# Kernel optimization log

Hardware: AMD Instinct MI355X
Metric: run time of the kernel (lower is better)

## Reference

```python
import jax, jax.numpy as jnp
import numpy as np

D_MODEL = 192
D_STATE = 128
D_CONV = 4
EXPAND = 2
D_INNER = EXPAND * D_MODEL            # 384
D_HALF = D_INNER // 2                 # 192 (x and z channel count)
DT_RANK = -(-D_MODEL // 16)           # ceil(192/16) = 12
B, H, W = 8, 32, 32


def serpentine(x):
    # flip every odd row along width: x (b, c, h, w)
    return x.at[:, :, 1::2, :].set(jnp.flip(x[:, :, 1::2, :], axis=3))


def causal_dwconv_silu(x, w):
    # x: (b, d, l), w: (d, k). Left-pad -> causal depthwise conv, then silu.
    k = w.shape[1]
    L = x.shape[-1]
    xp = jnp.pad(x, ((0, 0), (0, 0), (k - 1, 0)))
    y = jnp.zeros_like(x)
    for i in range(k):  # k=4, tiny fixed loop
        y = y + w[:, i][None, :, None] * xp[:, :, i:i + L]
    return jax.nn.silu(y)


def selective_scan(u, delta, A, Bm, Cm, Dp):
    # u, delta: (b, d, l); Bm, Cm: (b, n, l); A: (d, n); Dp: (d,)
    b, d, L = u.shape
    n = A.shape[1]

    def step(h, xs):
        u_t, dt_t, B_t, C_t = xs  # (b,d), (b,d), (b,n), (b,n)
        dA = jnp.exp(dt_t[:, :, None] * A)                      # (b,d,n)
        h = dA * h + (dt_t * u_t)[:, :, None] * B_t[:, None, :]
        y = jnp.einsum('bdn,bn->bd', h, C_t)
        return h, y

    xs = (jnp.moveaxis(u, 2, 0), jnp.moveaxis(delta, 2, 0),
          jnp.moveaxis(Bm, 2, 0), jnp.moveaxis(Cm, 2, 0))
    h0 = jnp.zeros((b, d, n), u.dtype)
    _, ys = jax.lax.scan(step, h0, xs)                          # (l, b, d)
    return jnp.moveaxis(ys, 0, 2).reshape(b, d, L) + Dp[None, :, None] * u


def setup_inputs() -> dict:
    key = jax.random.key(0)
    ks = jax.random.split(key, 8)
    hidden_states = jax.random.normal(ks[0], (B, D_MODEL, H, W), jnp.float32)
    W_in = jax.random.normal(ks[1], (D_INNER, D_MODEL), jnp.float32) * 0.02
    conv_w_x = jax.random.normal(ks[2], (D_HALF, D_CONV), jnp.float32) * 0.2
    conv_w_z = jax.random.normal(ks[3], (D_HALF, D_CONV), jnp.float32) * 0.2
    W_xproj = jax.random.normal(ks[4], (DT_RANK + 2 * D_STATE, D_HALF), jnp.float32) * 0.02
    dt_std = DT_RANK ** (-0.5)
    W_dt = jax.random.uniform(ks[5], (D_HALF, DT_RANK), jnp.float32, -dt_std, dt_std)
    # inv-softplus init of dt bias, as in the module
    dt = jnp.exp(jax.random.uniform(ks[6], (D_HALF,), jnp.float32)
                 * (np.log(0.1) - np.log(0.001)) + np.log(0.001))
    dt = jnp.clip(dt, 1e-4, None)
    b_dt = dt + jnp.log(-jnp.expm1(-dt))
    A_log = jnp.log(jnp.broadcast_to(jnp.arange(1, D_STATE + 1, dtype=jnp.float32),
                                     (D_HALF, D_STATE)))
    D_param = jnp.ones((D_HALF,), jnp.float32)
    W_out = jax.random.normal(ks[7], (D_MODEL, D_INNER), jnp.float32) * 0.02
    return {"hidden_states": hidden_states, "W_in": W_in, "conv_w_x": conv_w_x,
            "conv_w_z": conv_w_z, "W_xproj": W_xproj, "W_dt": W_dt, "b_dt": b_dt,
            "A_log": A_log, "D_param": D_param, "W_out": W_out}


def reference(hidden_states, W_in, conv_w_x, conv_w_z, W_xproj, W_dt, b_dt,
              A_log, D_param, W_out):
    b, c, h, w = hidden_states.shape
    L = h * w
    hs = serpentine(hidden_states)
    hs = hs.reshape(b, c, L).transpose(0, 2, 1)                 # (b, l, c)
    xz = hs @ W_in.T                                            # (b, l, 2d)
    xz = xz.transpose(0, 2, 1)                                  # (b, 2d, l)
    x, z = xz[:, :D_HALF], xz[:, D_HALF:]
    A = -jnp.exp(A_log.astype(jnp.float32))                     # (d, n)
    x = causal_dwconv_silu(x, conv_w_x)
    z = causal_dwconv_silu(z, conv_w_z)
    x_dbl = x.transpose(0, 2, 1) @ W_xproj.T                    # (b, l, r+2n)
    dt = x_dbl[..., :DT_RANK]
    Bm = x_dbl[..., DT_RANK:DT_RANK + D_STATE].transpose(0, 2, 1)  # (b, n, l)
    Cm = x_dbl[..., DT_RANK + D_STATE:].transpose(0, 2, 1)         # (b, n, l)
    dt = (dt @ W_dt.T + b_dt).transpose(0, 2, 1)                # (b, d, l), bias once
    # module passes delta_bias=dt_proj.bias again with delta_softplus=True
    delta = jax.nn.softplus(dt + b_dt[None, :, None])           # bias twice, faithful
    y = selective_scan(x, delta, A, Bm, Cm, D_param.astype(jnp.float32))
    y = jnp.concatenate([y, z], axis=1)                         # (b, 2d, l)
    out = y.transpose(0, 2, 1) @ W_out.T                        # (b, l, c)
    out = out.transpose(0, 2, 1).reshape(b, c, h, w)
    return serpentine(out)
```

## Files before the change

kernel.cpp:

```cpp
#include <hip/hip_runtime.h>
#include <math.h>

#define NB  8
#define DM  192
#define DH  192
#define DI  384
#define DS  128
#define DTR 12
#define XR  268
#define L   1024
#define NC  16
#define CL  64
#define NWX 320
#define LOG2E 1.44269504f

__device__ __forceinline__ void wave_lds_sync() {
  __builtin_amdgcn_wave_barrier();
  asm volatile("s_waitcnt lgkmcnt(0)" ::: "memory");
  __builtin_amdgcn_sched_barrier(0);
}

__global__ void k_wt_all(const float* __restrict__ Win,
                         const float* __restrict__ Wx,
                         const float* __restrict__ Wout,
                         float* __restrict__ wt_in,
                         float* __restrict__ wt_x,
                         float* __restrict__ wt_out) {
  const int j = blockIdx.x * 256 + threadIdx.x;
  const int k = blockIdx.y;
  const int z = blockIdx.z;
  if (z == 0) {
    if (k < 192 && j < 384) wt_in[(size_t)k * 384 + j] = Win[(size_t)j * 192 + k];
  } else if (z == 1) {
    if (k < 192 && j < NWX) wt_x[(size_t)k * NWX + j] = (j < XR) ? Wx[(size_t)j * 192 + k] : 0.f;
  } else {
    if (k < 384 && j < 192) wt_out[(size_t)k * 192 + j] = Wout[(size_t)j * 384 + k];
  }
}

template<int K, int N, int NW, int SERP_IN, int OMODE, int DODT>
__global__ __launch_bounds__(256) void k_gemm(const float* __restrict__ A,
                                              const float* __restrict__ Wt,
                                              float* __restrict__ Out,
                                              const float* __restrict__ Wdt,
                                              const float* __restrict__ bdt,
                                              float* __restrict__ dlt) {
  __shared__ float At[32][64];
  const int lane = threadIdx.x & 63;
  const int wv   = threadIdx.x >> 6;
  const int l    = blockIdx.x * 64 + lane;
  const int n0   = __builtin_amdgcn_readfirstlane(blockIdx.y * 64 + wv * 16);
  const int b    = blockIdx.z;
  int lg = l;
  if (SERP_IN || OMODE == 2) {
    int h = l >> 5, w = l & 31;
    lg = h * 32 + ((h & 1) ? (31 - w) : w);
  }
  const float* Ab = A + (size_t)b * K * L + (SERP_IN ? lg : l);
  float acc[16];
#pragma unroll
  for (int i = 0; i < 16; ++i) acc[i] = 0.f;

  for (int k0 = 0; k0 < K; k0 += 32) {
#pragma unroll
    for (int i = 0; i < 8; ++i) {
      int kr = wv * 8 + i;
      At[kr][lane] = Ab[(size_t)(k0 + kr) * L];
    }
    __syncthreads();
#pragma unroll
    for (int kk = 0; kk < 32; ++kk) {
      float a = At[kk][lane];
      const float* wr = Wt + (size_t)(k0 + kk) * NW + n0;
#pragma unroll
      for (int i = 0; i < 16; ++i) acc[i] = fmaf(wr[i], a, acc[i]);
    }
    __syncthreads();
  }

  if (OMODE == 0) {
    float* o = Out + ((size_t)b * N + n0) * L + l;
#pragma unroll
    for (int i = 0; i < 16; ++i) o[(size_t)i * L] = acc[i];
  } else if (OMODE == 1) {
    float* o = Out + ((size_t)b * L + l) * XR;
#pragma unroll
    for (int i = 0; i < 16; i += 4) {
      if (n0 + i + 4 <= XR)
        *(float4*)(o + n0 + i) = make_float4(acc[i], acc[i + 1], acc[i + 2], acc[i + 3]);
    }
    if (DODT && n0 == 0) {
      for (int d = 0; d < DH; ++d) {
        const float* wd = Wdt + d * DTR;
        float s = 2.f * bdt[d];
#pragma unroll
        for (int r = 0; r < DTR; ++r) s = fmaf(wd[r], acc[r], s);
        float v = (s > 20.f) ? s : __logf(1.f + __expf(s));
        dlt[((size_t)b * DH + d) * L + l] = v;
      }
    }
  } else {
    float* o = Out + ((size_t)b * N + n0) * L + lg;
#pragma unroll
    for (int i = 0; i < 16; ++i) o[(size_t)i * L] = acc[i];
  }
}

__global__ void k_conv_silu(const float* __restrict__ xz,
                            const float* __restrict__ cwx,
                            const float* __restrict__ cwz,
                            float* __restrict__ u,
                            float* __restrict__ ycat) {
  int idx = blockIdx.x * blockDim.x + threadIdx.x;
  const int per = NB * DH * (L / 4);
  int part = idx / per;
  int rem  = idx - part * per;
  int l4 = (rem & (L / 4 - 1)) * 4;
  int bd = rem >> 8;
  int d  = bd % DH;
  int b  = bd / DH;
  const float* cw = (part ? cwz : cwx) + d * 4;
  float w0 = cw[0], w1 = cw[1], w2 = cw[2], w3 = cw[3];
  const float* src = xz + ((size_t)b * DI + (part ? DH + d : d)) * L;
  float4 cur = *(const float4*)(src + l4);
  float pm3 = 0.f, pm2 = 0.f, pm1 = 0.f;
  if (l4 >= 4) {
    float4 p = *(const float4*)(src + l4 - 4);
    pm3 = p.y; pm2 = p.z; pm1 = p.w;
  }
  float s0 = fmaf(w3, cur.x, fmaf(w2, pm1,   fmaf(w1, pm2,   w0 * pm3)));
  float s1 = fmaf(w3, cur.y, fmaf(w2, cur.x, fmaf(w1, pm1,   w0 * pm2)));
  float s2 = fmaf(w3, cur.z, fmaf(w2, cur.y, fmaf(w1, cur.x, w0 * pm1)));
  float s3 = fmaf(w3, cur.w, fmaf(w2, cur.z, fmaf(w1, cur.y, w0 * cur.x)));
  float4 y;
  y.x = s0 / (1.f + __expf(-s0));
  y.y = s1 / (1.f + __expf(-s1));
  y.z = s2 / (1.f + __expf(-s2));
  y.w = s3 / (1.f + __expf(-s3));
  float* dst = part ? (ycat + ((size_t)b * DI + DH + d) * L + l4)
                    : (u + (size_t)bd * L + l4);
  *(float4*)dst = y;
}

__global__ void __launch_bounds__(256) k_scan1(const float* __restrict__ xdbl,
                                               const float* __restrict__ delta,
                                               const float* __restrict__ u,
                                               const float* __restrict__ Alog,
                                               float* __restrict__ hpart,
                                               float* __restrict__ apart) {
  __shared__ __align__(16) float dd[4][64][8];
  const int lane = threadIdx.x & 63;
  const int wv   = threadIdx.x >> 6;
  const int d0   = blockIdx.x * 8 + wv * 2;
  const int c = blockIdx.y, b = blockIdx.z;
  const int bd0 = b * DH + d0, bd1 = bd0 + 1;
  const float a00 = -__expf(Alog[(size_t)d0 * DS + 2 * lane]) * LOG2E;
  const float a10 = -__expf(Alog[(size_t)(d0 + 1) * DS + 2 * lane]) * LOG2E;
  const float* xrow  = xdbl + ((size_t)b * L + c * CL) * XR + DTR + 2 * lane;
  const float* drow0 = delta + (size_t)bd0 * L + c * CL;
  const float* drow1 = delta + (size_t)bd1 * L + c * CL;
  const float* urow0 = u + (size_t)bd0 * L + c * CL;
  const float* urow1 = u + (size_t)bd1 * L + c * CL;
  float dt0 = drow0[lane], u0 = urow0[lane];
  float dt1 = drow1[lane], u1 = urow1[lane];
  *(float4*)&dd[wv][lane][0] =
      make_float4(dt0, dt0 * u0, __builtin_amdgcn_exp2f(-dt0 * LOG2E), 0.f);
  *(float4*)&dd[wv][lane][4] =
      make_float4(dt1, dt1 * u1, __builtin_amdgcn_exp2f(-dt1 * LOG2E), 0.f);
  float s0 = dt0, s1 = dt1;
#pragma unroll
  for (int m = 1; m < 64; m <<= 1) {
    s0 += __shfl_xor(s0, m, 64);
    s1 += __shfl_xor(s1, m, 64);
  }
  wave_lds_sync();
  float h00 = 0.f, h01 = 0.f, h10 = 0.f, h11 = 0.f;
#pragma unroll 8
  for (int t = 0; t < CL; ++t) {
    float4 v0 = *(const float4*)&dd[wv][t][0];
    float4 v1 = *(const float4*)&dd[wv][t][4];
    float2 Bv = *(const float2*)(xrow + (size_t)t * XR);
    float e00 = __builtin_amdgcn_exp2f(v0.x * a00);
    float e01 = e00 * v0.z;
    float e10 = __builtin_amdgcn_exp2f(v1.x * a10);
    float e11 = e10 * v1.z;
    h00 = fmaf(e00, h00, v0.y * Bv.x);
    h01 = fmaf(e01, h01, v0.y * Bv.y);
    h10 = fmaf(e10, h10, v1.y * Bv.x);
    h11 = fmaf(e11, h11, v1.y * Bv.y);
  }
  float ap00 = __builtin_amdgcn_exp2f(s0 * a00);
  float ap01 = ap00 * __builtin_amdgcn_exp2f(-s0 * LOG2E);
  float ap10 = __builtin_amdgcn_exp2f(s1 * a10);
  float ap11 = ap10 * __builtin_amdgcn_exp2f(-s1 * LOG2E);
  *(float2*)(hpart + ((size_t)bd0 * NC + c) * 128 + 2 * lane) = make_float2(h00, h01);
  *(float2*)(hpart + ((size_t)bd1 * NC + c) * 128 + 2 * lane) = make_float2(h10, h11);
  *(float2*)(apart + ((size_t)bd0 * NC + c) * 128 + 2 * lane) = make_float2(ap00, ap01);
  *(float2*)(apart + ((size_t)bd1 * NC + c) * 128 + 2 * lane) = make_float2(ap10, ap11);
}

__global__ void __launch_bounds__(64) k_scan2(float* __restrict__ hpart,
                                              const float* __restrict__ apart) {
  const int bd   = blockIdx.x;
  const int lane = threadIdx.x;
  float H1 = 0.f, H2 = 0.f;
  size_t base = (size_t)bd * (NC * 128) + lane;
  for (int c = 0; c < NC; ++c) {
    size_t o = base + c * 128;
    float hp1 = hpart[o], hp2 = hpart[o + 64];
    float ap1 = apart[o], ap2 = apart[o + 64];
    hpart[o] = H1; hpart[o + 64] = H2;
    H1 = fmaf(ap1, H1, hp1);
    H2 = fmaf(ap2, H2, hp2);
  }
}

__global__ void __launch_bounds__(256) k_scan3(const float* __restrict__ xdbl,
                                               const float* __restrict__ delta,
                                               const float* __restrict__ u,
                                               const float* __restrict__ Alog,
                                               const float* __restrict__ Dp,
                                               const float* __restrict__ hin,
                                               float* __restrict__ ycat) {
  __shared__ __align__(16) float dd[4][64][8];
  __shared__ __align__(16) float pbuf[4][2][8][68];
  const int lane = threadIdx.x & 63;
  const int wv   = threadIdx.x >> 6;
  const int d0   = blockIdx.x * 8 + wv * 2;
  const int c = blockIdx.y, b = blockIdx.z;
  const int bd0 = b * DH + d0, bd1 = bd0 + 1;
  const float a00 = -__expf(Alog[(size_t)d0 * DS + 2 * lane]) * LOG2E;
  const float a10 = -__expf(Alog[(size_t)(d0 + 1) * DS + 2 * lane]) * LOG2E;
  const float* xrow  = xdbl + ((size_t)b * L + c * CL) * XR + DTR + 2 * lane;
  const float* drow0 = delta + (size_t)bd0 * L + c * CL;
  const float* drow1 = delta + (size_t)bd1 * L + c * CL;
  const float* urow0 = u + (size_t)bd0 * L + c * CL;
  const float* urow1 = u + (size_t)bd1 * L + c * CL;
  {
    float dt0 = drow0[lane], u0 = urow0[lane];
    float dt1 = drow1[lane], u1 = urow1[lane];
    *(float4*)&dd[wv][lane][0] =
        make_float4(dt0, dt0 * u0, __builtin_amdgcn_exp2f(-dt0 * LOG2E), 0.f);
    *(float4*)&dd[wv][lane][4] =
        make_float4(dt1, dt1 * u1, __builtin_amdgcn_exp2f(-dt1 * LOG2E), 0.f);
  }
  wave_lds_sync();
  const float* hp0 = hin + ((size_t)bd0 * NC + c) * 128 + 2 * lane;
  const float* hp1 = hin + ((size_t)bd1 * NC + c) * 128 + 2 * lane;
  float2 h0 = *(const float2*)hp0;
  float2 h1 = *(const float2*)hp1;
  const int ch = lane >> 5, pp = (lane >> 3) & 3, tl = lane & 7;
  float* yrow_my = ycat + ((size_t)b * DI + d0 + ch) * L + c * CL;
  const float* urow_my = ch ? urow1 : urow0;
  const float Dd_my = Dp[d0 + ch];

  float2 Br[8], Cr[8];
#pragma unroll
  for (int i = 0; i < 8; ++i) {
    Br[i] = *(const float2*)(xrow + (size_t)i * XR);
    Cr[i] = *(const float2*)(xrow + (size_t)i * XR + DS);
  }

  for (int t8 = 0; t8 < 8; ++t8) {
#pragma unroll
    for (int i = 0; i < 8; ++i) {
      const int t = t8 * 8 + i;
      float4 v0 = *(const float4*)&dd[wv][t][0];
      float4 v1 = *(const float4*)&dd[wv][t][4];
      float e00 = __builtin_amdgcn_exp2f(v0.x * a00);
      float e01 = e00 * v0.z;
      float e10 = __builtin_amdgcn_exp2f(v1.x * a10);
      float e11 = e10 * v1.z;
      h0.x = fmaf(e00, h0.x, v0.y * Br[i].x);
      h0.y = fmaf(e01, h0.y, v0.y * Br[i].y);
      h1.x = fmaf(e10, h1.x, v1.y * Br[i].x);
      h1.y = fmaf(e11, h1.y, v1.y * Br[i].y);
      pbuf[wv][0][i][lane] = fmaf(h0.y, Cr[i].y, h0.x * Cr[i].x);
      pbuf[wv][1][i][lane] = fmaf(h1.y, Cr[i].y, h1.x * Cr[i].x);
    }
    if (t8 < 7) {
#pragma unroll
      for (int i = 0; i < 8; ++i) {
        const int t = (t8 + 1) * 8 + i;
        Br[i] = *(const float2*)(xrow + (size_t)t * XR);
        Cr[i] = *(const float2*)(xrow + (size_t)t * XR + DS);
      }
    }
    wave_lds_sync();
    const float* pr = &pbuf[wv][ch][tl][pp * 16];
    float4 v0 = *(const float4*)(pr);
    float4 v1 = *(const float4*)(pr + 4);
    float4 v2 = *(const float4*)(pr + 8);
    float4 v3 = *(const float4*)(pr + 12);
    float s = (((v0.x + v0.y) + (v0.z + v0.w)) + ((v1.x + v1.y) + (v1.z + v1.w)))
            + (((v2.x + v2.y) + (v2.z + v2.w)) + ((v3.x + v3.y) + (v3.z + v3.w)));
    s += __shfl_xor(s, 8, 64);
    s += __shfl_xor(s, 16, 64);
    if (pp == 0) {
      const int t = t8 * 8 + tl;
      yrow_my[t] = fmaf(Dd_my, urow_my[t], s);
    }
    __builtin_amdgcn_wave_barrier();
  }
}

__global__ void __launch_bounds__(64) k_scan(const float* __restrict__ xdbl,
                                             const float* __restrict__ delta,
                                             const float* __restrict__ u,
                                             const float* __restrict__ Alog,
                                             const float* __restrict__ Dp,
                                             float* __restrict__ ycat) {
  const int bd   = blockIdx.x;
  const int b    = bd / DH;
  const int d    = bd % DH;
  const int lane = threadIdx.x;
  const float a1 = -__expf(Alog[d * DS + lane]);
  const float a2 = -__expf(Alog[d * DS + 64 + lane]);
  const float* xrow = xdbl + (size_t)b * L * XR;
  const float* drow = delta + (size_t)bd * L;
  const float* urow = u + (size_t)bd * L;
  const float Dd = Dp[d];
  float* yrow = ycat + ((size_t)b * DI + d) * L;
  float h1 = 0.f, h2 = 0.f;
  for (int t = 0; t < L; ++t) {
    const float* xd = xrow + (size_t)t * XR;
    float Bv1 = xd[DTR + lane];
    float Bv2 = xd[DTR + 64 + lane];
    float Cv1 = xd[DTR + DS + lane];
    float Cv2 = xd[DTR + DS + 64 + lane];
    float dt = drow[t];
    float ut = urow[t];
    float du = dt * ut;
    h1 = fmaf(__expf(dt * a1), h1, du * Bv1);
    h2 = fmaf(__expf(dt * a2), h2, du * Bv2);
    float p = fmaf(h2, Cv2, h1 * Cv1);
#pragma unroll
    for (int m = 32; m; m >>= 1) p += __shfl_xor(p, m, 64);
    if (lane == 0) yrow[t] = fmaf(Dd, ut, p);
  }
}

extern "C" void kernel_launch(void* const* d_in, const int* in_sizes, int n_in,
                              void* d_out, int out_size, void* d_ws, size_t ws_size,
                              hipStream_t stream) {
  const float* hid  = (const float*)d_in[0];
  const float* Win  = (const float*)d_in[1];
  const float* cwx  = (const float*)d_in[2];
  const float* cwz  = (const float*)d_in[3];
  const float* Wx   = (const float*)d_in[4];
  const float* Wdt  = (const float*)d_in[5];
  const float* bdt  = (const float*)d_in[6];
  const float* Alog = (const float*)d_in[7];
  const float* Dp   = (const float*)d_in[8];
  const float* Wout = (const float*)d_in[9];
  float* out = (float*)d_out;

  float* ws    = (float*)d_ws;
  float* xz    = ws;
  float* u     = xz   + (size_t)NB * DI * L;
  float* ycat  = u    + (size_t)NB * DH * L;
  float* xdbl  = ycat + (size_t)NB * DI * L;
  float* delta = xdbl + (size_t)NB * L * XR;
  float* apart = delta + (size_t)NB * DH * L;
  float* wt_in = apart + (size_t)NB * DH * NC * 128;
  float* wt_x  = wt_in + (size_t)192 * 384;
  float* wt_out= wt_x  + (size_t)192 * NWX;
  float* hpart = xz;

  const size_t need = ((size_t)NB * DI * L * 2 + (size_t)NB * DH * L * 2 +
                       (size_t)NB * L * XR + (size_t)NB * DH * NC * 128 +
                       (size_t)192 * 384 + (size_t)192 * NWX + (size_t)384 * 192) * 4;

  k_wt_all<<<dim3(2, 384, 3), dim3(256), 0, stream>>>(Win, Wx, Wout, wt_in, wt_x, wt_out);

  k_gemm<192, 384, 384, 1, 0, 0><<<dim3(16, 6, NB), dim3(256), 0, stream>>>(
      hid, wt_in, xz, nullptr, nullptr, nullptr);
  k_conv_silu<<<dim3(2 * NB * DH * (L / 4) / 256), dim3(256), 0, stream>>>(xz, cwx, cwz, u, ycat);
  k_gemm<192, XR, NWX, 0, 1, 1><<<dim3(16, 5, NB), dim3(256), 0, stream>>>(
      u, wt_x, xdbl, Wdt, bdt, delta);

  if (ws_size >= need) {
    k_scan1<<<dim3(DH / 8, NC, NB), dim3(256), 0, stream>>>(xdbl, delta, u, Alog, hpart, apart);
    k_scan2<<<dim3(NB * DH), dim3(64), 0, stream>>>(hpart, apart);
    k_scan3<<<dim3(DH / 8, NC, NB), dim3(256), 0, stream>>>(xdbl, delta, u, Alog, Dp, hpart, ycat);
  } else {
    k_scan<<<dim3(NB * DH), dim3(64), 0, stream>>>(xdbl, delta, u, Alog, Dp, ycat);
  }

  k_gemm<384, 192, 192, 0, 2, 0><<<dim3(16, 3, NB), dim3(256), 0, stream>>>(
      ycat, wt_out, out, nullptr, nullptr, nullptr);
}
```

Measured before the change: 213.8 us.

## Halve GEMM output tile per block and spread dt projection across waves

Each GEMM block now computes 32 output columns instead of 64 (8 accumulators per wave), which doubles the grid along y for all three projection GEMMs. The LDS staging tile is re-laid out so each lane reads four k-values with one float4 load. The dt-projection plus softplus, previously done serially over all 192 channels by a single wave, now has its 12 rank values shared through LDS and is split across four waves of 48 channels each. The aim is more parallelism and a shorter serial tail, at the cost of reading the A operand twice as often overall.

```diff
diff --git a/kernel.cpp b/kernel.cpp
--- a/kernel.cpp
+++ b/kernel.cpp
@@ -45,11 +45,12 @@
                                               const float* __restrict__ Wdt,
                                               const float* __restrict__ bdt,
                                               float* __restrict__ dlt) {
-  __shared__ float At[32][64];
+  __shared__ __align__(16) float At2[8][64][4];
+  __shared__ float xdl[DODT ? 64 * 13 : 1];
   const int lane = threadIdx.x & 63;
   const int wv   = threadIdx.x >> 6;
   const int l    = blockIdx.x * 64 + lane;
-  const int n0   = __builtin_amdgcn_readfirstlane(blockIdx.y * 64 + wv * 16);
+  const int n0   = __builtin_amdgcn_readfirstlane(blockIdx.y * 32 + wv * 8);
   const int b    = blockIdx.z;
   int lg = l;
   if (SERP_IN || OMODE == 2) {
@@ -57,23 +58,28 @@
     lg = h * 32 + ((h & 1) ? (31 - w) : w);
   }
   const float* Ab = A + (size_t)b * K * L + (SERP_IN ? lg : l);
-  float acc[16];
-#pragma unroll
-  for (int i = 0; i < 16; ++i) acc[i] = 0.f;
+  float acc[8];
+#pragma unroll
+  for (int i = 0; i < 8; ++i) acc[i] = 0.f;
 
   for (int k0 = 0; k0 < K; k0 += 32) {
 #pragma unroll
     for (int i = 0; i < 8; ++i) {
       int kr = wv * 8 + i;
-      At[kr][lane] = Ab[(size_t)(k0 + kr) * L];
+      At2[kr >> 2][lane][kr & 3] = Ab[(size_t)(k0 + kr) * L];
     }
     __syncthreads();
 #pragma unroll
-    for (int kk = 0; kk < 32; ++kk) {
-      float a = At[kk][lane];
-      const float* wr = Wt + (size_t)(k0 + kk) * NW + n0;
-#pragma unroll
-      for (int i = 0; i < 16; ++i) acc[i] = fmaf(wr[i], a, acc[i]);
+    for (int kk4 = 0; kk4 < 8; ++kk4) {
+      float4 a4 = *(const float4*)&At2[kk4][lane][0];
+      float av[4] = {a4.x, a4.y, a4.z, a4.w};
+#pragma unroll
+      for (int j = 0; j < 4; ++j) {
+        const float* wr = Wt + (size_t)(k0 + kk4 * 4 + j) * NW + n0;
+        float a = av[j];
+#pragma unroll
+        for (int i = 0; i < 8; ++i) acc[i] = fmaf(wr[i], a, acc[i]);
+      }
     }
     __syncthreads();
   }
@@ -81,28 +87,43 @@
   if (OMODE == 0) {
     float* o = Out + ((size_t)b * N + n0) * L + l;
 #pragma unroll
-    for (int i = 0; i < 16; ++i) o[(size_t)i * L] = acc[i];
+    for (int i = 0; i < 8; ++i) o[(size_t)i * L] = acc[i];
   } else if (OMODE == 1) {
     float* o = Out + ((size_t)b * L + l) * XR;
 #pragma unroll
-    for (int i = 0; i < 16; i += 4) {
+    for (int i = 0; i < 8; i += 4) {
       if (n0 + i + 4 <= XR)
         *(float4*)(o + n0 + i) = make_float4(acc[i], acc[i + 1], acc[i + 2], acc[i + 3]);
     }
-    if (DODT && n0 == 0) {
-      for (int d = 0; d < DH; ++d) {
+  } else {
+    float* o = Out + ((size_t)b * N + n0) * L + lg;
+#pragma unroll
+    for (int i = 0; i < 8; ++i) o[(size_t)i * L] = acc[i];
+  }
+
+  if constexpr (DODT) {
+    if (blockIdx.y == 0) {
+      if (wv == 0) {
+#pragma unroll
+        for (int i = 0; i < 8; ++i) xdl[lane * 13 + i] = acc[i];
+      } else if (wv == 1) {
+#pragma unroll
+        for (int i = 0; i < 4; ++i) xdl[lane * 13 + 8 + i] = acc[i];
+      }
+      __syncthreads();
+      float x[12];
+#pragma unroll
+      for (int r = 0; r < 12; ++r) x[r] = xdl[lane * 13 + r];
+      const int dlo = wv * 48;
+      for (int d = dlo; d < dlo + 48; ++d) {
         const float* wd = Wdt + d * DTR;
         float s = 2.f * bdt[d];
 #pragma unroll
-        for (int r = 0; r < DTR; ++r) s = fmaf(wd[r], acc[r], s);
+        for (int r = 0; r < DTR; ++r) s = fmaf(wd[r], x[r], s);
         float v = (s > 20.f) ? s : __logf(1.f + __expf(s));
         dlt[((size_t)b * DH + d) * L + l] = v;
       }
     }
-  } else {
-    float* o = Out + ((size_t)b * N + n0) * L + lg;
-#pragma unroll
-    for (int i = 0; i < 16; ++i) o[(size_t)i * L] = acc[i];
   }
 }
 
@@ -373,10 +394,10 @@
 
   k_wt_all<<<dim3(2, 384, 3), dim3(256), 0, stream>>>(Win, Wx, Wout, wt_in, wt_x, wt_out);
 
-  k_gemm<192, 384, 384, 1, 0, 0><<<dim3(16, 6, NB), dim3(256), 0, stream>>>(
+  k_gemm<192, 384, 384, 1, 0, 0><<<dim3(16, 12, NB), dim3(256), 0, stream>>>(
       hid, wt_in, xz, nullptr, nullptr, nullptr);
   k_conv_silu<<<dim3(2 * NB * DH * (L / 4) / 256), dim3(256), 0, stream>>>(xz, cwx, cwz, u, ycat);
-  k_gemm<192, XR, NWX, 0, 1, 1><<<dim3(16, 5, NB), dim3(256), 0, stream>>>(
+  k_gemm<192, XR, NWX, 0, 1, 1><<<dim3(16, 10, NB), dim3(256), 0, stream>>>(
       u, wt_x, xdbl, Wdt, bdt, delta);
 
   if (ws_size >= need) {
@@ -387,6 +408,6 @@
     k_scan<<<dim3(NB * DH), dim3(64), 0, stream>>>(xdbl, delta, u, Alog, Dp, ycat);
   }
 
-  k_gemm<384, 192, 192, 0, 2, 0><<<dim3(16, 3, NB), dim3(256), 0, stream>>>(
+  k_gemm<384, 192, 192, 0, 2, 0><<<dim3(16, 6, NB), dim3(256), 0, stream>>>(
       ycat, wt_out, out, nullptr, nullptr, nullptr);
 }
```

After: 202.9 us. 1.05x faster.
